# Optimization experiments

Hardware: AMD Instinct MI355X
Metric: run time of the kernel (lower is better)

The kernel has to match this reference:

```python
import jax, jax.numpy as jnp
import numpy as np
import math

B, S, D, H = 2, 2048, 1024, 16
DK = D // H


def setup_inputs() -> dict:
    key = jax.random.key(0)
    ks = jax.random.split(key, 12)
    s = 1.0 / math.sqrt(D)
    inp = {
        "q": jax.random.normal(ks[0], (B, S, D), jnp.float32),
        "k": jax.random.normal(ks[1], (B, S, D), jnp.float32),
        "v": jax.random.normal(ks[2], (B, S, D), jnp.float32),
        "mask": jnp.broadcast_to(jnp.tril(jnp.ones((S, S), jnp.int32))[None, None], (B, 1, S, S)),
        "Wq": jax.random.normal(ks[3], (D, D), jnp.float32) * s,
        "bq": jnp.zeros((D,), jnp.float32),
        "Wk": jax.random.normal(ks[4], (D, D), jnp.float32) * s,
        "bk": jnp.zeros((D,), jnp.float32),
        "Wv": jax.random.normal(ks[5], (D, D), jnp.float32) * s,
        "bv": jnp.zeros((D,), jnp.float32),
        "Wo": jax.random.normal(ks[6], (D, D), jnp.float32) * s,
        "bo": jnp.zeros((D,), jnp.float32),
    }
    return inp


def reference(q, k, v, mask, Wq, bq, Wk, bk, Wv, bv, Wo, bo):
    b = q.shape[0]
    # project and split heads -> [b, h, s, d_k]
    def heads(x, W, bias):
        y = x @ W.T + bias
        return y.reshape(b, -1, H, DK).transpose(0, 2, 1, 3)
    qh = heads(q, Wq, bq)
    kh = heads(k, Wk, bk)
    vh = heads(v, Wv, bv)
    scores = jnp.einsum("bhqd,bhkd->bhqk", qh, kh) / math.sqrt(DK)
    scores = jnp.where(mask == 0, jnp.float32(-1e9), scores)
    weights = jax.nn.softmax(scores, axis=-1)  # dropout p=0 -> identity
    out = jnp.einsum("bhqk,bhkd->bhqd", weights, vh)
    out = out.transpose(0, 2, 1, 3).reshape(b, -1, H * DK)
    return out @ Wo.T + bo
```

## Files before the change

kernel.cpp:

```cpp
#include <hip/hip_runtime.h>

#define B_ 2
#define S_ 2048
#define D_ 1024
#define H_ 16
#define DK_ 64
#define M_ 4096

typedef unsigned short u16;
typedef __bf16 bf16x8 __attribute__((ext_vector_type(8)));
typedef float floatx4 __attribute__((ext_vector_type(4)));

#if __has_builtin(__builtin_amdgcn_exp2f)
#define EXP2F(x) __builtin_amdgcn_exp2f(x)
#else
#define EXP2F(x) exp2f(x)
#endif

__device__ __forceinline__ u16 f2bf(float f) {
  unsigned u = __float_as_uint(f);
  u += 0x7fffu + ((u >> 16) & 1u);
  return (u16)(u >> 16);
}

__device__ __forceinline__ void stage16(const void* g, void* l) {
  __builtin_amdgcn_global_load_lds(
      (const __attribute__((address_space(1))) unsigned int*)g,
      (__attribute__((address_space(3))) unsigned int*)l, 16, 0, 0);
}

__global__ __launch_bounds__(256) void cvt_all_kernel(
    const float* __restrict__ q, const float* __restrict__ k, const float* __restrict__ v,
    const float* __restrict__ wq, const float* __restrict__ wk,
    const float* __restrict__ wv, const float* __restrict__ wo,
    u16* dq, u16* dk, u16* dv, u16* dwq, u16* dwk, u16* dwv, u16* dwo) {
  const float* s; u16* d; size_t base;
  const int bx = blockIdx.x;
  if (bx < 6144) {
    const int t0 = bx >> 11;
    base = (size_t)(bx & 2047) * 2048;
    s = t0 == 0 ? q : t0 == 1 ? k : v;
    d = t0 == 0 ? dq : t0 == 1 ? dk : dv;
  } else {
    const int t0 = (bx - 6144) >> 9;
    base = (size_t)((bx - 6144) & 511) * 2048;
    s = t0 == 0 ? wq : t0 == 1 ? wk : t0 == 2 ? wv : wo;
    d = t0 == 0 ? dwq : t0 == 1 ? dwk : t0 == 2 ? dwv : dwo;
  }
  const size_t i = base + (size_t)threadIdx.x * 8;
  const float4 f0 = *reinterpret_cast<const float4*>(s + i);
  const float4 f1 = *reinterpret_cast<const float4*>(s + i + 4);
  union { u16 h[8]; uint4 u; } cv;
  cv.h[0] = f2bf(f0.x); cv.h[1] = f2bf(f0.y); cv.h[2] = f2bf(f0.z); cv.h[3] = f2bf(f0.w);
  cv.h[4] = f2bf(f1.x); cv.h[5] = f2bf(f1.y); cv.h[6] = f2bf(f1.z); cv.h[7] = f2bf(f1.w);
  *reinterpret_cast<uint4*>(d + i) = cv.u;
}

template <int BN>
__device__ __forceinline__ void gemm_body(
    const u16* __restrict__ A, const u16* __restrict__ W,
    const float* __restrict__ bias, void* __restrict__ outp,
    int mode, float scale) {
  constexpr int NT = BN / 32;
  constexpr int NBI = BN / 64;
  __shared__ __align__(16) u16 As[2][128 * 32];
  __shared__ __align__(16) u16 Bs[2][BN * 32];

  const int t = threadIdx.x;
  const int lane = t & 63, w = t >> 6;
  const int quad = lane >> 4, l16 = lane & 15;
  const int wm = w >> 1, wn = w & 1;
  const int m0 = blockIdx.x * 128, n0 = blockIdx.y * BN;

  const int sp = lane >> 3, ssw = lane & 7, sc = ssw ^ sp;
  const u16 *gA[2], *gB[NBI]; u16 *lA[2], *lB[NBI];
#pragma unroll
  for (int i = 0; i < 2; i++) {
    const int ri = i * 4 + w;
    gA[i] = A + (size_t)(m0 + ri * 16 + 2 * sp + (sc >> 2)) * 1024 + (sc & 3) * 8;
    lA[i] = As[0] + ri * 64 * 8;
  }
#pragma unroll
  for (int i = 0; i < NBI; i++) {
    const int ri = i * 4 + w;
    gB[i] = W + (size_t)(n0 + ri * 16 + 2 * sp + (sc >> 2)) * 1024 + (sc & 3) * 8;
    lB[i] = Bs[0] + ri * 64 * 8;
  }

  floatx4 acc[4][NT] = {};

#pragma unroll
  for (int i = 0; i < 2; i++) stage16(gA[i], lA[i]);
#pragma unroll
  for (int i = 0; i < NBI; i++) stage16(gB[i], lB[i]);

  for (int k0 = 0; k0 < 1024; k0 += 32) {
    const int cur = (k0 >> 5) & 1, nxt = cur ^ 1;
    __syncthreads();
    if (k0 + 32 < 1024) {
#pragma unroll
      for (int i = 0; i < 2; i++) stage16(gA[i] + k0 + 32, lA[i] + nxt * 128 * 32);
#pragma unroll
      for (int i = 0; i < NBI; i++) stage16(gB[i] + k0 + 32, lB[i] + nxt * BN * 32);
    }
    bf16x8 af[4], bf[NT];
#pragma unroll
    for (int mt = 0; mt < 4; mt++) {
      const int row = wm * 64 + mt * 16 + l16;
      const int pg = row >> 1;
      const int sw = (((row & 1) << 2) | quad) ^ (pg & 7);
      af[mt] = *reinterpret_cast<const bf16x8*>(&As[cur][(pg * 8 + sw) * 8]);
    }
#pragma unroll
    for (int nt = 0; nt < NT; nt++) {
      const int row = wn * (NT * 16) + nt * 16 + l16;
      const int pg = row >> 1;
      const int sw = (((row & 1) << 2) | quad) ^ (pg & 7);
      bf[nt] = *reinterpret_cast<const bf16x8*>(&Bs[cur][(pg * 8 + sw) * 8]);
    }
#pragma unroll
    for (int mt = 0; mt < 4; mt++)
#pragma unroll
      for (int nt = 0; nt < NT; nt++)
        acc[mt][nt] = __builtin_amdgcn_mfma_f32_16x16x32_bf16(af[mt], bf[nt], acc[mt][nt], 0, 0, 0);
  }

#pragma unroll
  for (int mt = 0; mt < 4; mt++) {
    const int mbase = m0 + wm * 64 + mt * 16 + quad * 4;
    const int bb = mbase >> 11, s0v = mbase & 2047;
#pragma unroll
    for (int nt = 0; nt < NT; nt++) {
      const int n = n0 + wn * (NT * 16) + nt * 16 + l16;
      const float bvv = bias[n];
      if (mode == 0) {
        u16* Y = (u16*)outp;
        const int h = n >> 6, dk = n & 63;
#pragma unroll
        for (int r = 0; r < 4; r++)
          Y[(((size_t)(bb * H_ + h)) * S_ + (s0v + r)) * DK_ + dk] =
              f2bf((acc[mt][nt][r] + bvv) * scale);
      } else if (mode == 2) {
        u16* Y = (u16*)outp;
        const int h = n >> 6, dk = n & 63;
        union { u16 h4[4]; uint2 u; } pk2;
#pragma unroll
        for (int r = 0; r < 4; r++) pk2.h4[r] = f2bf(acc[mt][nt][r] + bvv);
        *reinterpret_cast<uint2*>(
            &Y[(((size_t)(bb * H_ + h)) * DK_ + dk) * S_ + s0v]) = pk2.u;
      } else {
        float* Y = (float*)outp;
#pragma unroll
        for (int r = 0; r < 4; r++)
          Y[(size_t)(mbase + r) * 1024 + n] = acc[mt][nt][r] + bvv;
      }
    }
  }
}

__global__ __launch_bounds__(256) void qkv_gemm_kernel(
    const u16* qa, const u16* ka, const u16* va,
    const u16* wq, const u16* wk, const u16* wv,
    const float* bq, const float* bk, const float* bv,
    u16* Qh, u16* Kh, u16* VhT) {
  const int g = blockIdx.z;
  const u16* A = g == 0 ? qa : g == 1 ? ka : va;
  const u16* W = g == 0 ? wq : g == 1 ? wk : wv;
  const float* bias = g == 0 ? bq : g == 1 ? bk : bv;
  void* out = g == 0 ? (void*)Qh : g == 1 ? (void*)Kh : (void*)VhT;
  gemm_body<128>(A, W, bias, out, g == 2 ? 2 : 0,
                 g == 0 ? 0.18033688011112f : 1.0f);
}

__global__ __launch_bounds__(256) void o_gemm_kernel(
    const u16* ctx, const u16* wo, const float* bo, float* out) {
  gemm_body<64>(ctx, wo, bo, out, 3, 1.0f);
}

__global__ __launch_bounds__(256) void attn_kernel(
    const u16* __restrict__ Qh, const u16* __restrict__ Kh,
    const u16* __restrict__ VhT, u16* __restrict__ Ctx) {
  __shared__ __align__(16) u16 Kt[64 * 64];
  __shared__ __align__(16) u16 Vt[64 * 64];
  __shared__ __align__(16) u16 Ps[64 * 72];

  const int t = threadIdx.x;
  const int lane = t & 63, w = t >> 6;
  const int quad = lane >> 4, l16 = lane & 15;

  const int bh = blockIdx.x & 31;
  const int i = blockIdx.x >> 5;
  const int j = i >> 3, r0 = i & 7;
  const int u = (j == 0) ? 31 - r0 : (j == 1) ? r0 : (j == 2) ? 23 - r0 : 8 + r0;
  const int qb = u * 64;
  const int ntile = u + 1;

  const u16* Qp = Qh + (size_t)bh * S_ * DK_;
  const u16* Kp = Kh + (size_t)bh * S_ * DK_;
  const u16* Vp = VhT + (size_t)bh * DK_ * S_;

  bf16x8 bq[2];
#pragma unroll
  for (int kk = 0; kk < 2; kk++)
    bq[kk] = *reinterpret_cast<const bf16x8*>(
        &Qp[(size_t)(qb + w * 16 + l16) * DK_ + kk * 32 + quad * 8]);

  const u16 *gK[2], *gV[2]; u16 *lK[2], *lV[2];
#pragma unroll
  for (int i2 = 0; i2 < 2; i2++) {
    const int ch = (i2 * 4 + w) * 64 + lane;
    const int row = ch >> 3, c = ch & 7, cs = c ^ (row & 7);
    gK[i2] = Kp + (size_t)row * DK_ + cs * 8;
    gV[i2] = Vp + (size_t)row * S_ + cs * 8;
    lK[i2] = Kt + ((i2 * 4 + w) * 64) * 8;
    lV[i2] = Vt + ((i2 * 4 + w) * 64) * 8;
  }

  float l_run = 0.f;
  floatx4 o[4] = {};
  const int qg = qb + w * 16 + l16;

  for (int it = 0; it < ntile; it++) {
    const int j0 = it * 64;
#pragma unroll
    for (int i2 = 0; i2 < 2; i2++) {
      stage16(gK[i2] + (size_t)j0 * DK_, lK[i2]);
      stage16(gV[i2] + j0, lV[i2]);
    }
    __syncthreads();

    floatx4 sc[4] = {};
#pragma unroll
    for (int mt = 0; mt < 4; mt++) {
      const int row = mt * 16 + l16;
#pragma unroll
      for (int kk = 0; kk < 2; kk++) {
        const bf16x8 ak = *reinterpret_cast<const bf16x8*>(
            &Kt[(row * 8 + ((kk * 4 + quad) ^ (l16 & 7))) * 8]);
        sc[mt] = __builtin_amdgcn_mfma_f32_16x16x32_bf16(ak, bq[kk], sc[mt], 0, 0, 0);
      }
    }

    const bool maskT = (it == ntile - 1);
    float psum = 0.f;
#pragma unroll
    for (int mt = 0; mt < 4; mt++) {
      float p[4];
#pragma unroll
      for (int r = 0; r < 4; r++) {
        float vsc = sc[mt][r];
        if (maskT && (j0 + mt * 16 + quad * 4 + r > qg)) vsc = -1e30f;
        p[r] = EXP2F(vsc);
        psum += p[r];
      }
      uint2 pu;
      pu.x = (__float_as_uint(p[1]) & 0xffff0000u) | (__float_as_uint(p[0]) >> 16);
      pu.y = (__float_as_uint(p[3]) & 0xffff0000u) | (__float_as_uint(p[2]) >> 16);
      *reinterpret_cast<uint2*>(&Ps[(w * 16 + l16) * 72 + mt * 16 + quad * 4]) = pu;
    }
    psum += __shfl_xor(psum, 16);
    psum += __shfl_xor(psum, 32);
    l_run += psum;

#pragma unroll
    for (int kk = 0; kk < 2; kk++) {
      const bf16x8 ap = *reinterpret_cast<const bf16x8*>(
          &Ps[(w * 16 + l16) * 72 + kk * 32 + quad * 8]);
#pragma unroll
      for (int nt = 0; nt < 4; nt++) {
        const bf16x8 bv = *reinterpret_cast<const bf16x8*>(
            &Vt[((nt * 16 + l16) * 8 + ((kk * 4 + quad) ^ (l16 & 7))) * 8]);
        o[nt] = __builtin_amdgcn_mfma_f32_16x16x32_bf16(ap, bv, o[nt], 0, 0, 0);
      }
    }
    __syncthreads();
  }

  const int bb = bh >> 4, hh = bh & 15;
#pragma unroll
  for (int r = 0; r < 4; r++) {
    const float lr = __shfl(l_run, quad * 4 + r);
    const float inv = 1.0f / lr;
    const int srow = qb + w * 16 + quad * 4 + r;
    u16* cp = Ctx + ((size_t)bb * S_ + srow) * D_ + hh * DK_;
#pragma unroll
    for (int nt = 0; nt < 4; nt++)
      cp[nt * 16 + l16] = f2bf(o[nt][r] * inv);
  }
}

extern "C" void kernel_launch(void* const* d_in, const int* in_sizes, int n_in,
                              void* d_out, int out_size, void* d_ws, size_t ws_size,
                              hipStream_t stream) {
  const float* q  = (const float*)d_in[0];
  const float* k  = (const float*)d_in[1];
  const float* v  = (const float*)d_in[2];
  const float* Wq = (const float*)d_in[4];
  const float* bq = (const float*)d_in[5];
  const float* Wk = (const float*)d_in[6];
  const float* bk = (const float*)d_in[7];
  const float* Wv = (const float*)d_in[8];
  const float* bv = (const float*)d_in[9];
  const float* Wo = (const float*)d_in[10];
  const float* bo = (const float*)d_in[11];

  const size_t nW = (size_t)D_ * D_;
  const size_t nA = (size_t)M_ * D_;
  u16* wqb = (u16*)d_ws;
  u16* wkb = wqb + nW;
  u16* wvb = wkb + nW;
  u16* wob = wvb + nW;
  u16* qb_ = wob + nW;
  u16* kb_ = qb_ + nA;
  u16* vb_ = kb_ + nA;
  u16* Qh  = vb_ + nA;
  u16* Kh  = Qh + nA;
  u16* VhT = Kh + nA;
  u16* Ctx = qb_;

  cvt_all_kernel<<<dim3(8192), 256, 0, stream>>>(q, k, v, Wq, Wk, Wv, Wo,
                                                 qb_, kb_, vb_, wqb, wkb, wvb, wob);

  qkv_gemm_kernel<<<dim3(M_ / 128, D_ / 128, 3), 256, 0, stream>>>(
      qb_, kb_, vb_, wqb, wkb, wvb, bq, bk, bv, Qh, Kh, VhT);

  attn_kernel<<<dim3(B_ * H_ * (S_ / 64)), 256, 0, stream>>>(Qh, Kh, VhT, Ctx);

  o_gemm_kernel<<<dim3(M_ / 128, D_ / 64), 256, 0, stream>>>(Ctx, wob, bo, (float*)d_out);
}
```

Before: 241.1 us.

## Fuse all MHA stages into one cooperative persistent kernel with grid syncs

Replaces the four separate launches (convert, QKV GEMM, attention, output GEMM) with one cooperative kernel of 1024 blocks that runs each stage in turn and separates them with grid-wide syncs. Along the way the conversion does 8 chunks per block, the QKV GEMM tile drops to 128x64 with some blocks taking two jobs, and the output GEMM uses 64x64 tiles. The goal is to remove launch gaps and tail effects between kernels. In exchange there are grid barrier costs, the load imbalance of doing 1536 QKV jobs on 1024 blocks, and a co-residency requirement of four blocks per CU. If the cooperative launch fails, it falls back to separate kernels.

```diff
diff --git a/kernel.cpp b/kernel.cpp
--- a/kernel.cpp
+++ b/kernel.cpp
@@ -1,4 +1,7 @@
 #include <hip/hip_runtime.h>
+#include <hip/hip_cooperative_groups.h>
+
+namespace cg = cooperative_groups;
 
 #define B_ 2
 #define S_ 2048
@@ -29,68 +32,71 @@
       (__attribute__((address_space(3))) unsigned int*)l, 16, 0, 0);
 }
 
-__global__ __launch_bounds__(256) void cvt_all_kernel(
-    const float* __restrict__ q, const float* __restrict__ k, const float* __restrict__ v,
-    const float* __restrict__ wq, const float* __restrict__ wk,
-    const float* __restrict__ wv, const float* __restrict__ wo,
+__device__ __forceinline__ void cvt_phase(
+    int bx, const float* q, const float* k, const float* v,
+    const float* Wq, const float* Wk, const float* Wv, const float* Wo,
     u16* dq, u16* dk, u16* dv, u16* dwq, u16* dwk, u16* dwv, u16* dwo) {
-  const float* s; u16* d; size_t base;
-  const int bx = blockIdx.x;
-  if (bx < 6144) {
-    const int t0 = bx >> 11;
-    base = (size_t)(bx & 2047) * 2048;
+  const float* s; u16* d; int slice;
+  if (bx < 768) {
+    const int t0 = bx >> 8;
     s = t0 == 0 ? q : t0 == 1 ? k : v;
     d = t0 == 0 ? dq : t0 == 1 ? dk : dv;
+    slice = bx & 255;
   } else {
-    const int t0 = (bx - 6144) >> 9;
-    base = (size_t)((bx - 6144) & 511) * 2048;
-    s = t0 == 0 ? wq : t0 == 1 ? wk : t0 == 2 ? wv : wo;
+    const int t0 = (bx - 768) >> 6;
+    s = t0 == 0 ? Wq : t0 == 1 ? Wk : t0 == 2 ? Wv : Wo;
     d = t0 == 0 ? dwq : t0 == 1 ? dwk : t0 == 2 ? dwv : dwo;
-  }
-  const size_t i = base + (size_t)threadIdx.x * 8;
-  const float4 f0 = *reinterpret_cast<const float4*>(s + i);
-  const float4 f1 = *reinterpret_cast<const float4*>(s + i + 4);
-  union { u16 h[8]; uint4 u; } cv;
-  cv.h[0] = f2bf(f0.x); cv.h[1] = f2bf(f0.y); cv.h[2] = f2bf(f0.z); cv.h[3] = f2bf(f0.w);
-  cv.h[4] = f2bf(f1.x); cv.h[5] = f2bf(f1.y); cv.h[6] = f2bf(f1.z); cv.h[7] = f2bf(f1.w);
-  *reinterpret_cast<uint4*>(d + i) = cv.u;
-}
-
-template <int BN>
-__device__ __forceinline__ void gemm_body(
-    const u16* __restrict__ A, const u16* __restrict__ W,
+    slice = (bx - 768) & 63;
+  }
+  const size_t base = (size_t)slice * 16384 + (size_t)threadIdx.x * 8;
+#pragma unroll
+  for (int it = 0; it < 8; it++) {
+    const size_t i = base + (size_t)it * 2048;
+    const float4 f0 = *reinterpret_cast<const float4*>(s + i);
+    const float4 f1 = *reinterpret_cast<const float4*>(s + i + 4);
+    union { u16 h[8]; uint4 u; } cv;
+    cv.h[0] = f2bf(f0.x); cv.h[1] = f2bf(f0.y); cv.h[2] = f2bf(f0.z); cv.h[3] = f2bf(f0.w);
+    cv.h[4] = f2bf(f1.x); cv.h[5] = f2bf(f1.y); cv.h[6] = f2bf(f1.z); cv.h[7] = f2bf(f1.w);
+    *reinterpret_cast<uint4*>(d + i) = cv.u;
+  }
+}
+
+template <int BM, int BN>
+__device__ __forceinline__ void gemm_phase(
+    u16* smem, const u16* __restrict__ A, const u16* __restrict__ W,
     const float* __restrict__ bias, void* __restrict__ outp,
-    int mode, float scale) {
+    int mode, float scale, int m0, int n0) {
+  constexpr int MT = BM / 32;
   constexpr int NT = BN / 32;
+  constexpr int NAI = BM / 64;
   constexpr int NBI = BN / 64;
-  __shared__ __align__(16) u16 As[2][128 * 32];
-  __shared__ __align__(16) u16 Bs[2][BN * 32];
+  u16* As = smem;
+  u16* Bs = smem + 2 * BM * 32;
 
   const int t = threadIdx.x;
   const int lane = t & 63, w = t >> 6;
   const int quad = lane >> 4, l16 = lane & 15;
   const int wm = w >> 1, wn = w & 1;
-  const int m0 = blockIdx.x * 128, n0 = blockIdx.y * BN;
 
   const int sp = lane >> 3, ssw = lane & 7, sc = ssw ^ sp;
-  const u16 *gA[2], *gB[NBI]; u16 *lA[2], *lB[NBI];
-#pragma unroll
-  for (int i = 0; i < 2; i++) {
+  const u16 *gA[NAI], *gB[NBI]; u16 *lA[NAI], *lB[NBI];
+#pragma unroll
+  for (int i = 0; i < NAI; i++) {
     const int ri = i * 4 + w;
     gA[i] = A + (size_t)(m0 + ri * 16 + 2 * sp + (sc >> 2)) * 1024 + (sc & 3) * 8;
-    lA[i] = As[0] + ri * 64 * 8;
+    lA[i] = As + ri * 64 * 8;
   }
 #pragma unroll
   for (int i = 0; i < NBI; i++) {
     const int ri = i * 4 + w;
     gB[i] = W + (size_t)(n0 + ri * 16 + 2 * sp + (sc >> 2)) * 1024 + (sc & 3) * 8;
-    lB[i] = Bs[0] + ri * 64 * 8;
-  }
-
-  floatx4 acc[4][NT] = {};
-
-#pragma unroll
-  for (int i = 0; i < 2; i++) stage16(gA[i], lA[i]);
+    lB[i] = Bs + ri * 64 * 8;
+  }
+
+  floatx4 acc[MT][NT] = {};
+
+#pragma unroll
+  for (int i = 0; i < NAI; i++) stage16(gA[i], lA[i]);
 #pragma unroll
   for (int i = 0; i < NBI; i++) stage16(gB[i], lB[i]);
 
@@ -99,39 +105,39 @@
     __syncthreads();
     if (k0 + 32 < 1024) {
 #pragma unroll
-      for (int i = 0; i < 2; i++) stage16(gA[i] + k0 + 32, lA[i] + nxt * 128 * 32);
+      for (int i = 0; i < NAI; i++) stage16(gA[i] + k0 + 32, lA[i] + nxt * BM * 32);
 #pragma unroll
       for (int i = 0; i < NBI; i++) stage16(gB[i] + k0 + 32, lB[i] + nxt * BN * 32);
     }
-    bf16x8 af[4], bf[NT];
-#pragma unroll
-    for (int mt = 0; mt < 4; mt++) {
-      const int row = wm * 64 + mt * 16 + l16;
+    bf16x8 af[MT], bf[NT];
+#pragma unroll
+    for (int mt = 0; mt < MT; mt++) {
+      const int row = wm * (BM / 2) + mt * 16 + l16;
       const int pg = row >> 1;
       const int sw = (((row & 1) << 2) | quad) ^ (pg & 7);
-      af[mt] = *reinterpret_cast<const bf16x8*>(&As[cur][(pg * 8 + sw) * 8]);
+      af[mt] = *reinterpret_cast<const bf16x8*>(&As[cur * BM * 32 + (pg * 8 + sw) * 8]);
     }
 #pragma unroll
     for (int nt = 0; nt < NT; nt++) {
-      const int row = wn * (NT * 16) + nt * 16 + l16;
+      const int row = wn * (BN / 2) + nt * 16 + l16;
       const int pg = row >> 1;
       const int sw = (((row & 1) << 2) | quad) ^ (pg & 7);
-      bf[nt] = *reinterpret_cast<const bf16x8*>(&Bs[cur][(pg * 8 + sw) * 8]);
-    }
-#pragma unroll
-    for (int mt = 0; mt < 4; mt++)
+      bf[nt] = *reinterpret_cast<const bf16x8*>(&Bs[cur * BN * 32 + (pg * 8 + sw) * 8]);
+    }
+#pragma unroll
+    for (int mt = 0; mt < MT; mt++)
 #pragma unroll
       for (int nt = 0; nt < NT; nt++)
         acc[mt][nt] = __builtin_amdgcn_mfma_f32_16x16x32_bf16(af[mt], bf[nt], acc[mt][nt], 0, 0, 0);
   }
 
 #pragma unroll
-  for (int mt = 0; mt < 4; mt++) {
-    const int mbase = m0 + wm * 64 + mt * 16 + quad * 4;
+  for (int mt = 0; mt < MT; mt++) {
+    const int mbase = m0 + wm * (BM / 2) + mt * 16 + quad * 4;
     const int bb = mbase >> 11, s0v = mbase & 2047;
 #pragma unroll
     for (int nt = 0; nt < NT; nt++) {
-      const int n = n0 + wn * (NT * 16) + nt * 16 + l16;
+      const int n = n0 + wn * (BN / 2) + nt * 16 + l16;
       const float bvv = bias[n];
       if (mode == 0) {
         u16* Y = (u16*)outp;
@@ -158,38 +164,34 @@
   }
 }
 
-__global__ __launch_bounds__(256) void qkv_gemm_kernel(
-    const u16* qa, const u16* ka, const u16* va,
-    const u16* wq, const u16* wk, const u16* wv,
+__device__ __forceinline__ void qkv_job(
+    u16* smem, int j, const u16* qb_, const u16* kb_, const u16* vb_,
+    const u16* wqb, const u16* wkb, const u16* wvb,
     const float* bq, const float* bk, const float* bv,
     u16* Qh, u16* Kh, u16* VhT) {
-  const int g = blockIdx.z;
-  const u16* A = g == 0 ? qa : g == 1 ? ka : va;
-  const u16* W = g == 0 ? wq : g == 1 ? wk : wv;
-  const float* bias = g == 0 ? bq : g == 1 ? bk : bv;
-  void* out = g == 0 ? (void*)Qh : g == 1 ? (void*)Kh : (void*)VhT;
-  gemm_body<128>(A, W, bias, out, g == 2 ? 2 : 0,
-                 g == 0 ? 0.18033688011112f : 1.0f);
-}
-
-__global__ __launch_bounds__(256) void o_gemm_kernel(
-    const u16* ctx, const u16* wo, const float* bo, float* out) {
-  gemm_body<64>(ctx, wo, bo, out, 3, 1.0f);
-}
-
-__global__ __launch_bounds__(256) void attn_kernel(
-    const u16* __restrict__ Qh, const u16* __restrict__ Kh,
-    const u16* __restrict__ VhT, u16* __restrict__ Ctx) {
-  __shared__ __align__(16) u16 Kt[64 * 64];
-  __shared__ __align__(16) u16 Vt[64 * 64];
-  __shared__ __align__(16) u16 Ps[64 * 72];
+  const int g = j >> 9, r = j & 511;
+  const int m0 = (r & 31) * 128, n0 = (r >> 5) * 64;
+  if (g == 0)
+    gemm_phase<128, 64>(smem, qb_, wqb, bq, Qh, 0, 0.18033688011112f, m0, n0);
+  else if (g == 1)
+    gemm_phase<128, 64>(smem, kb_, wkb, bk, Kh, 0, 1.0f, m0, n0);
+  else
+    gemm_phase<128, 64>(smem, vb_, wvb, bv, VhT, 2, 1.0f, m0, n0);
+}
+
+__device__ __forceinline__ void attn_phase(
+    u16* smem, const u16* __restrict__ Qh, const u16* __restrict__ Kh,
+    const u16* __restrict__ VhT, u16* __restrict__ Ctx, int bx) {
+  u16* Kt = smem;
+  u16* Vt = smem + 4096;
+  u16* Ps = smem + 8192;
 
   const int t = threadIdx.x;
   const int lane = t & 63, w = t >> 6;
   const int quad = lane >> 4, l16 = lane & 15;
 
-  const int bh = blockIdx.x & 31;
-  const int i = blockIdx.x >> 5;
+  const int bh = bx & 31;
+  const int i = bx >> 5;
   const int j = i >> 3, r0 = i & 7;
   const int u = (j == 0) ? 31 - r0 : (j == 1) ? r0 : (j == 2) ? 23 - r0 : 8 + r0;
   const int qb = u * 64;
@@ -199,10 +201,10 @@
   const u16* Kp = Kh + (size_t)bh * S_ * DK_;
   const u16* Vp = VhT + (size_t)bh * DK_ * S_;
 
-  bf16x8 bq[2];
+  bf16x8 bqf[2];
 #pragma unroll
   for (int kk = 0; kk < 2; kk++)
-    bq[kk] = *reinterpret_cast<const bf16x8*>(
+    bqf[kk] = *reinterpret_cast<const bf16x8*>(
         &Qp[(size_t)(qb + w * 16 + l16) * DK_ + kk * 32 + quad * 8]);
 
   const u16 *gK[2], *gV[2]; u16 *lK[2], *lV[2];
@@ -237,7 +239,7 @@
       for (int kk = 0; kk < 2; kk++) {
         const bf16x8 ak = *reinterpret_cast<const bf16x8*>(
             &Kt[(row * 8 + ((kk * 4 + quad) ^ (l16 & 7))) * 8]);
-        sc[mt] = __builtin_amdgcn_mfma_f32_16x16x32_bf16(ak, bq[kk], sc[mt], 0, 0, 0);
+        sc[mt] = __builtin_amdgcn_mfma_f32_16x16x32_bf16(ak, bqf[kk], sc[mt], 0, 0, 0);
       }
     }
 
@@ -287,6 +289,76 @@
     for (int nt = 0; nt < 4; nt++)
       cp[nt * 16 + l16] = f2bf(o[nt][r] * inv);
   }
+}
+
+__global__ void __launch_bounds__(256, 4) fused_mha_kernel(
+    const float* q, const float* k, const float* v,
+    const float* Wq, const float* bq, const float* Wk, const float* bk,
+    const float* Wv, const float* bv, const float* Wo, const float* bo,
+    u16* ws, float* out) {
+  __shared__ __align__(16) u16 smem[16384];
+  const int bx = blockIdx.x;
+
+  const size_t nW = (size_t)D_ * D_;
+  const size_t nA = (size_t)M_ * D_;
+  u16* wqb = ws;
+  u16* wkb = wqb + nW;
+  u16* wvb = wkb + nW;
+  u16* wob = wvb + nW;
+  u16* qb_ = wob + nW;
+  u16* kb_ = qb_ + nA;
+  u16* vb_ = kb_ + nA;
+  u16* Qh  = vb_ + nA;
+  u16* Kh  = Qh + nA;
+  u16* VhT = Kh + nA;
+  u16* Ctx = qb_;
+
+  cvt_phase(bx, q, k, v, Wq, Wk, Wv, Wo, qb_, kb_, vb_, wqb, wkb, wvb, wob);
+  __threadfence();
+  cg::this_grid().sync();
+
+  qkv_job(smem, bx, qb_, kb_, vb_, wqb, wkb, wvb, bq, bk, bv, Qh, Kh, VhT);
+  if (bx < 512)
+    qkv_job(smem, 1024 + bx, qb_, kb_, vb_, wqb, wkb, wvb, bq, bk, bv, Qh, Kh, VhT);
+  __threadfence();
+  cg::this_grid().sync();
+
+  attn_phase(smem, Qh, Kh, VhT, Ctx, bx);
+  __threadfence();
+  cg::this_grid().sync();
+
+  gemm_phase<64, 64>(smem, Ctx, wob, bo, out, 3, 1.0f,
+                     (bx & 63) * 64, (bx >> 6) * 64);
+}
+
+__global__ __launch_bounds__(256) void cvt_fb(
+    const float* q, const float* k, const float* v,
+    const float* Wq, const float* Wk, const float* Wv, const float* Wo,
+    u16* dq, u16* dk, u16* dv, u16* dwq, u16* dwk, u16* dwv, u16* dwo) {
+  cvt_phase(blockIdx.x, q, k, v, Wq, Wk, Wv, Wo, dq, dk, dv, dwq, dwk, dwv, dwo);
+}
+
+__global__ __launch_bounds__(256) void qkv_fb(
+    const u16* qa, const u16* ka, const u16* va,
+    const u16* wq, const u16* wk, const u16* wv,
+    const float* bq, const float* bk, const float* bv,
+    u16* Qh, u16* Kh, u16* VhT) {
+  __shared__ __align__(16) u16 smem[12288];
+  const int j = blockIdx.z * 512 + blockIdx.y * 32 + blockIdx.x;
+  qkv_job(smem, j, qa, ka, va, wq, wk, wv, bq, bk, bv, Qh, Kh, VhT);
+}
+
+__global__ __launch_bounds__(256) void attn_fb(
+    const u16* Qh, const u16* Kh, const u16* VhT, u16* Ctx) {
+  __shared__ __align__(16) u16 smem[12800];
+  attn_phase(smem, Qh, Kh, VhT, Ctx, blockIdx.x);
+}
+
+__global__ __launch_bounds__(256) void o_fb(
+    const u16* ctx, const u16* wo, const float* bo, float* out) {
+  __shared__ __align__(16) u16 smem[8192];
+  gemm_phase<64, 64>(smem, ctx, wo, bo, out, 3, 1.0f,
+                     blockIdx.x * 64, blockIdx.y * 64);
 }
 
 extern "C" void kernel_launch(void* const* d_in, const int* in_sizes, int n_in,
@@ -303,28 +375,38 @@
   const float* bv = (const float*)d_in[9];
   const float* Wo = (const float*)d_in[10];
   const float* bo = (const float*)d_in[11];
-
-  const size_t nW = (size_t)D_ * D_;
-  const size_t nA = (size_t)M_ * D_;
-  u16* wqb = (u16*)d_ws;
-  u16* wkb = wqb + nW;
-  u16* wvb = wkb + nW;
-  u16* wob = wvb + nW;
-  u16* qb_ = wob + nW;
-  u16* kb_ = qb_ + nA;
-  u16* vb_ = kb_ + nA;
-  u16* Qh  = vb_ + nA;
-  u16* Kh  = Qh + nA;
-  u16* VhT = Kh + nA;
-  u16* Ctx = qb_;
-
-  cvt_all_kernel<<<dim3(8192), 256, 0, stream>>>(q, k, v, Wq, Wk, Wv, Wo,
-                                                 qb_, kb_, vb_, wqb, wkb, wvb, wob);
-
-  qkv_gemm_kernel<<<dim3(M_ / 128, D_ / 128, 3), 256, 0, stream>>>(
-      qb_, kb_, vb_, wqb, wkb, wvb, bq, bk, bv, Qh, Kh, VhT);
-
-  attn_kernel<<<dim3(B_ * H_ * (S_ / 64)), 256, 0, stream>>>(Qh, Kh, VhT, Ctx);
-
-  o_gemm_kernel<<<dim3(M_ / 128, D_ / 64), 256, 0, stream>>>(Ctx, wob, bo, (float*)d_out);
-}
+  u16* ws = (u16*)d_ws;
+  float* out = (float*)d_out;
+
+  void* args[] = {
+      (void*)&q, (void*)&k, (void*)&v,
+      (void*)&Wq, (void*)&bq, (void*)&Wk, (void*)&bk,
+      (void*)&Wv, (void*)&bv, (void*)&Wo, (void*)&bo,
+      (void*)&ws, (void*)&out};
+  hipError_t err = hipLaunchCooperativeKernel((void*)fused_mha_kernel,
+                                              dim3(1024), dim3(256),
+                                              args, 0, stream);
+  if (err != hipSuccess) {
+    (void)hipGetLastError();
+    const size_t nW = (size_t)D_ * D_;
+    const size_t nA = (size_t)M_ * D_;
+    u16* wqb = ws;
+    u16* wkb = wqb + nW;
+    u16* wvb = wkb + nW;
+    u16* wob = wvb + nW;
+    u16* qb_ = wob + nW;
+    u16* kb_ = qb_ + nA;
+    u16* vb_ = kb_ + nA;
+    u16* Qh  = vb_ + nA;
+    u16* Kh  = Qh + nA;
+    u16* VhT = Kh + nA;
+    u16* Ctx = qb_;
+
+    cvt_fb<<<dim3(1024), 256, 0, stream>>>(q, k, v, Wq, Wk, Wv, Wo,
+                                           qb_, kb_, vb_, wqb, wkb, wvb, wob);
+    qkv_fb<<<dim3(32, 16, 3), 256, 0, stream>>>(
+        qb_, kb_, vb_, wqb, wkb, wvb, bq, bk, bv, Qh, Kh, VhT);
+    attn_fb<<<dim3(1024), 256, 0, stream>>>(Qh, Kh, VhT, Ctx);
+    o_fb<<<dim3(64, 16), 256, 0, stream>>>(Ctx, wob, bo, out);
+  }
+}
```

New measurement: 953.0 us. +295.2%, slower.

## Split long causal attention rows into two KV partitions with combine kernel

Applied to the files above, without the earlier changes.

Query tiles whose causal KV range exceeds 16 tiles are split into two blocks, each covering half the KV range. The partial unnormalised outputs (bf16) and row sums go to workspace, and a new combine kernel adds and normalises them. The aim is to balance per-block work and shorten the longest blocks' tail latency. In exchange it adds an extra launch, extra global traffic, and bf16 rounding of the partial outputs. Max subtraction is not used, so summing the partials stays exact in form.

```diff
diff --git a/kernel.cpp b/kernel.cpp
--- a/kernel.cpp
+++ b/kernel.cpp
@@ -179,7 +179,8 @@
 
 __global__ __launch_bounds__(256) void attn_kernel(
     const u16* __restrict__ Qh, const u16* __restrict__ Kh,
-    const u16* __restrict__ VhT, u16* __restrict__ Ctx) {
+    const u16* __restrict__ VhT, u16* __restrict__ Ctx,
+    u16* __restrict__ po, float* __restrict__ pl) {
   __shared__ __align__(16) u16 Kt[64 * 64];
   __shared__ __align__(16) u16 Vt[64 * 64];
   __shared__ __align__(16) u16 Ps[64 * 72];
@@ -189,20 +190,28 @@
   const int quad = lane >> 4, l16 = lane & 15;
 
   const int bh = blockIdx.x & 31;
-  const int i = blockIdx.x >> 5;
-  const int j = i >> 3, r0 = i & 7;
-  const int u = (j == 0) ? 31 - r0 : (j == 1) ? r0 : (j == 2) ? 23 - r0 : 8 + r0;
+  const int cidx = blockIdx.x >> 5;
+  int u, part;
+  if (cidx < 17)       { u = 15 + cidx; part = 0; }
+  else if (cidx == 17) { u = 31;        part = 1; }
+  else {
+    const int k2 = cidx - 18, tt = 15 - (k2 >> 1);
+    if ((k2 & 1) == 0) { u = tt - 1;  part = 0; }
+    else               { u = tt + 15; part = 1; }
+  }
   const int qb = u * 64;
-  const int ntile = u + 1;
+  const bool twopart = (u >= 16);
+  const int tbeg = (part == 1) ? 16 : 0;
+  const int tend = (twopart && part == 0) ? 16 : u + 1;
 
   const u16* Qp = Qh + (size_t)bh * S_ * DK_;
   const u16* Kp = Kh + (size_t)bh * S_ * DK_;
   const u16* Vp = VhT + (size_t)bh * DK_ * S_;
 
-  bf16x8 bq[2];
+  bf16x8 bqf[2];
 #pragma unroll
   for (int kk = 0; kk < 2; kk++)
-    bq[kk] = *reinterpret_cast<const bf16x8*>(
+    bqf[kk] = *reinterpret_cast<const bf16x8*>(
         &Qp[(size_t)(qb + w * 16 + l16) * DK_ + kk * 32 + quad * 8]);
 
   const u16 *gK[2], *gV[2]; u16 *lK[2], *lV[2];
@@ -220,7 +229,7 @@
   floatx4 o[4] = {};
   const int qg = qb + w * 16 + l16;
 
-  for (int it = 0; it < ntile; it++) {
+  for (int it = tbeg; it < tend; it++) {
     const int j0 = it * 64;
 #pragma unroll
     for (int i2 = 0; i2 < 2; i2++) {
@@ -237,11 +246,11 @@
       for (int kk = 0; kk < 2; kk++) {
         const bf16x8 ak = *reinterpret_cast<const bf16x8*>(
             &Kt[(row * 8 + ((kk * 4 + quad) ^ (l16 & 7))) * 8]);
-        sc[mt] = __builtin_amdgcn_mfma_f32_16x16x32_bf16(ak, bq[kk], sc[mt], 0, 0, 0);
+        sc[mt] = __builtin_amdgcn_mfma_f32_16x16x32_bf16(ak, bqf[kk], sc[mt], 0, 0, 0);
       }
     }
 
-    const bool maskT = (it == ntile - 1);
+    const bool maskT = (it == u);
     float psum = 0.f;
 #pragma unroll
     for (int mt = 0; mt < 4; mt++) {
@@ -276,16 +285,52 @@
     __syncthreads();
   }
 
+  if (!twopart) {
+    const int bb = bh >> 4, hh = bh & 15;
+#pragma unroll
+    for (int r = 0; r < 4; r++) {
+      const float lr = __shfl(l_run, quad * 4 + r);
+      const float inv = 1.0f / lr;
+      const int srow = qb + w * 16 + quad * 4 + r;
+      u16* cp = Ctx + ((size_t)bb * S_ + srow) * D_ + hh * DK_;
+#pragma unroll
+      for (int nt = 0; nt < 4; nt++)
+        cp[nt * 16 + l16] = f2bf(o[nt][r] * inv);
+    }
+  } else {
+    u16* pob = po + ((((size_t)part * 32 + bh) * 16 + (u - 16)) * 64) * 64;
+#pragma unroll
+    for (int r = 0; r < 4; r++) {
+      const int row = w * 16 + quad * 4 + r;
+#pragma unroll
+      for (int nt = 0; nt < 4; nt++)
+        pob[row * 64 + nt * 16 + l16] = f2bf(o[nt][r]);
+    }
+    if (quad == 0)
+      pl[(((size_t)part * 32 + bh) * 16 + (u - 16)) * 64 + w * 16 + l16] = l_run;
+  }
+}
+
+__global__ __launch_bounds__(256) void combine_kernel(
+    const u16* __restrict__ po, const float* __restrict__ pl,
+    u16* __restrict__ Ctx) {
+  const int b = blockIdx.x;
+  const int bh = b & 31, ui = b >> 5;
+  const int t = threadIdx.x;
+  const int row = t >> 2, cg = (t & 3) * 16;
+  const float l = pl[(((size_t)0 * 32 + bh) * 16 + ui) * 64 + row] +
+                  pl[(((size_t)1 * 32 + bh) * 16 + ui) * 64 + row];
+  const float inv = 1.0f / l;
+  const u16* p0 = po + ((((size_t)0 * 32 + bh) * 16 + ui) * 64 + row) * 64 + cg;
+  const u16* p1 = po + ((((size_t)1 * 32 + bh) * 16 + ui) * 64 + row) * 64 + cg;
   const int bb = bh >> 4, hh = bh & 15;
-#pragma unroll
-  for (int r = 0; r < 4; r++) {
-    const float lr = __shfl(l_run, quad * 4 + r);
-    const float inv = 1.0f / lr;
-    const int srow = qb + w * 16 + quad * 4 + r;
-    u16* cp = Ctx + ((size_t)bb * S_ + srow) * D_ + hh * DK_;
-#pragma unroll
-    for (int nt = 0; nt < 4; nt++)
-      cp[nt * 16 + l16] = f2bf(o[nt][r] * inv);
+  const int s = (16 + ui) * 64 + row;
+  u16* cp = Ctx + ((size_t)bb * S_ + s) * D_ + hh * DK_ + cg;
+#pragma unroll
+  for (int j2 = 0; j2 < 16; j2++) {
+    const float v0 = __uint_as_float((unsigned)p0[j2] << 16);
+    const float v1 = __uint_as_float((unsigned)p1[j2] << 16);
+    cp[j2] = f2bf((v0 + v1) * inv);
   }
 }
 
@@ -317,6 +362,8 @@
   u16* Kh  = Qh + nA;
   u16* VhT = Kh + nA;
   u16* Ctx = qb_;
+  u16* po  = kb_;
+  float* pl = (float*)(VhT + nA);
 
   cvt_all_kernel<<<dim3(8192), 256, 0, stream>>>(q, k, v, Wq, Wk, Wv, Wo,
                                                  qb_, kb_, vb_, wqb, wkb, wvb, wob);
@@ -324,7 +371,9 @@
   qkv_gemm_kernel<<<dim3(M_ / 128, D_ / 128, 3), 256, 0, stream>>>(
       qb_, kb_, vb_, wqb, wkb, wvb, bq, bk, bv, Qh, Kh, VhT);
 
-  attn_kernel<<<dim3(B_ * H_ * (S_ / 64)), 256, 0, stream>>>(Qh, Kh, VhT, Ctx);
+  attn_kernel<<<dim3(1536), 256, 0, stream>>>(Qh, Kh, VhT, Ctx, po, pl);
+
+  combine_kernel<<<dim3(512), 256, 0, stream>>>(po, pl, Ctx);
 
   o_gemm_kernel<<<dim3(M_ / 128, D_ / 64), 256, 0, stream>>>(Ctx, wob, bo, (float*)d_out);
 }
```

Measured after the change: 234.2 us. -2.9%, faster.
